# Kernel optimization log

Measured on AMD Instinct MI355X. Metric: run time of the kernel, lower is better.

The kernel has to match this reference:

```python
import jax, jax.numpy as jnp
import numpy as np

N_NODES = 20000   # N
N_EDGES = 320000  # E (avg degree 16)
T_STEPS = 16      # T
IN_FEATS = 1      # F
HG = 64           # hidden_g
HT = 128          # hidden_t
LN_EPS = 1e-5


def _layer_norm(x, g, b):
    mu = jnp.mean(x, axis=-1, keepdims=True)
    var = jnp.mean((x - mu) ** 2, axis=-1, keepdims=True)
    return (x - mu) * jax.lax.rsqrt(var + LN_EPS) * g + b


def setup_inputs() -> dict:
    key = jax.random.key(0)
    k = jax.random.split(key, 16)
    r = lambda i, shape, s: jax.random.normal(k[i], shape, jnp.float32) * s
    return dict(
        x_seq=jax.random.normal(k[0], (1, T_STEPS, N_NODES, IN_FEATS), jnp.float32),
        edge_index=jax.random.randint(k[1], (2, N_EDGES), 0, N_NODES, dtype=jnp.int32),
        # SAGEConv layer 0: lin_l (aggregated neighbors, has bias) + lin_r (root)
        W_l0=r(2, (IN_FEATS, HG), 0.5), W_r0=r(3, (IN_FEATS, HG), 0.5), b0=jnp.zeros((HG,), jnp.float32),
        ln0_g=jnp.ones((HG,), jnp.float32), ln0_b=jnp.zeros((HG,), jnp.float32),
        # SAGEConv layer 1
        W_l1=r(4, (HG, HG), 0.1), W_r1=r(5, (HG, HG), 0.1), b1=jnp.zeros((HG,), jnp.float32),
        ln1_g=jnp.ones((HG,), jnp.float32), ln1_b=jnp.zeros((HG,), jnp.float32),
        # GRU (torch layout: gates r,z,n stacked along first dim)
        gru_Wih=r(6, (3 * HT, HG), 0.05), gru_Whh=r(7, (3 * HT, HT), 0.05),
        gru_bih=jnp.zeros((3 * HT,), jnp.float32), gru_bhh=jnp.zeros((3 * HT,), jnp.float32),
        # head
        head_W=r(8, (HT, 1), 0.05), head_b=jnp.zeros((1,), jnp.float32),
    )


def reference(x_seq, edge_index, W_l0, W_r0, b0, ln0_g, ln0_b,
              W_l1, W_r1, b1, ln1_g, ln1_b,
              gru_Wih, gru_Whh, gru_bih, gru_bhh, head_W, head_b):
    src, dst = edge_index[0], edge_index[1]
    # in-degree for mean aggregation (clamped to 1, like PyG mean aggr on isolated nodes)
    deg = jnp.clip(jax.ops.segment_sum(jnp.ones((N_EDGES,), jnp.float32), dst,
                                       num_segments=N_NODES), 1.0)[:, None]

    def sage(x, Wl, Wr, b):
        # mean over incoming neighbors, then lin_l(aggr) + lin_r(root)
        agg = jax.ops.segment_sum(x[src], dst, num_segments=N_NODES) / deg
        return agg @ Wl + x @ Wr + b

    def stack(xt):  # xt: (N, F) -> (N, HG); dropout is identity in eval mode
        h = jax.nn.relu(_layer_norm(sage(xt, W_l0, W_r0, b0), ln0_g, ln0_b))
        h = jax.nn.relu(_layer_norm(sage(h, W_l1, W_r1, b1), ln1_g, ln1_b))
        return h

    X = x_seq[0]  # (T, N, F), B == 1
    # scan over timesteps (matches the per-t Python loop, bounds peak memory)
    _, H = jax.lax.scan(lambda c, xt: (c, stack(xt)), None, X)  # H: (T, N, HG)

    def gru_step(h, xt):  # torch GRU cell; batch = N nodes
        gi = xt @ gru_Wih.T + gru_bih
        gh = h @ gru_Whh.T + gru_bhh
        ir, iz, inn = jnp.split(gi, 3, axis=-1)
        hr, hz, hn = jnp.split(gh, 3, axis=-1)
        r = jax.nn.sigmoid(ir + hr)
        z = jax.nn.sigmoid(iz + hz)
        n = jnp.tanh(inn + r * hn)
        return (1.0 - z) * n + z * h, None

    h0 = jnp.zeros((N_NODES, HT), x_seq.dtype)
    hT, _ = jax.lax.scan(gru_step, h0, H)
    y = (hT @ head_W + head_b)[:, 0]  # (N,)
    return y
```

## Files before the change

### kernel.cpp

```cpp
#include <hip/hip_runtime.h>
#include <math.h>

#define NN 20000
#define NE 320000
#define TS 16
#define HG 64
#define HTT 128
#define NG 384
#define LN_EPS 1e-5f
#define ASTR 1032

typedef __attribute__((ext_vector_type(8))) _Float16 f16x8;
typedef __attribute__((ext_vector_type(4))) float f32x4;

__device__ __forceinline__ float wave_sum64(float v) {
  #pragma unroll
  for (int off = 32; off > 0; off >>= 1) v += __shfl_xor(v, off, 64);
  return v;
}
__device__ __forceinline__ float quad_sum16(float v) {
  #pragma unroll
  for (int off = 1; off < 16; off <<= 1) v += __shfl_xor(v, off, 64);
  return v;
}
__device__ __forceinline__ float fast_sigmoid(float x) {
  return __builtin_amdgcn_rcpf(1.f + __expf(-x));
}
__device__ __forceinline__ float fast_tanh(float x) {
  float e = __expf(-2.f * fabsf(x));
  float th = (1.f - e) * __builtin_amdgcn_rcpf(1.f + e);
  return copysignf(th, x);
}

__global__ void k_init(int* cnt) {
  int i = blockIdx.x * blockDim.x + threadIdx.x;
  if (i < NN) cnt[i] = 0;
}

__global__ void k_hist(const int* __restrict__ dst, int* cnt) {
  int e = blockIdx.x * blockDim.x + threadIdx.x;
  if (e < NE) atomicAdd(&cnt[dst[e]], 1);
}

__global__ void k_scan(int* cnt, int* row_ptr, float* deg_inv) {
  __shared__ int s[1024];
  const int PER = 20;
  int tid = threadIdx.x;
  int base = tid * PER;
  int vloc[PER], dloc[PER];
  int sum = 0;
  #pragma unroll
  for (int j = 0; j < PER; j++) {
    int n = base + j;
    int d = (n < NN) ? cnt[n] : 0;
    vloc[j] = sum;
    dloc[j] = d;
    sum += d;
  }
  s[tid] = sum;
  __syncthreads();
  for (int off = 1; off < 1024; off <<= 1) {
    int t = (tid >= off) ? s[tid - off] : 0;
    __syncthreads();
    s[tid] += t;
    __syncthreads();
  }
  int excl = s[tid] - sum;
  #pragma unroll
  for (int j = 0; j < PER; j++) {
    int n = base + j;
    if (n < NN) {
      int rp = excl + vloc[j];
      row_ptr[n] = rp;
      cnt[n] = rp;
      int d = dloc[j];
      deg_inv[n] = 1.0f / (float)((d > 1) ? d : 1);
    }
  }
  if (tid == 1023) row_ptr[NN] = s[1023];
}

__global__ void k_fill(const int* __restrict__ src, const int* __restrict__ dst,
                       int* cursor, int* col) {
  int e = blockIdx.x * blockDim.x + threadIdx.x;
  if (e < NE) {
    int p = atomicAdd(&cursor[dst[e]], 1);
    col[p] = src[e];
  }
}

__global__ void k_cvt_f16(const float* __restrict__ w, _Float16* __restrict__ o, int n) {
  int i = blockIdx.x * blockDim.x + threadIdx.x;
  if (i < n) o[i] = (_Float16)w[i];
}

__global__ void k_cvt_sagef16(const float* __restrict__ Wl1, const float* __restrict__ Wr1,
                              _Float16* __restrict__ hi, _Float16* __restrict__ lo) {
  int i = blockIdx.x * blockDim.x + threadIdx.x;
  if (i < HG * 128) {
    int n = i >> 7, k = i & 127;
    float x = (k < HG) ? Wl1[k * HG + n] : Wr1[(k - HG) * HG + n];
    _Float16 h = (_Float16)x;
    hi[i] = h;
    lo[i] = (_Float16)(x - (float)h);
  }
}

__global__ void k_moments(const float* __restrict__ Wl0, const float* __restrict__ Wr0,
                          const float* __restrict__ b0, const float* __restrict__ g0,
                          const float* __restrict__ be0, float* __restrict__ P) {
  int f = threadIdx.x;
  float u = Wl0[f], v = Wr0[f], c = b0[f], g = g0[f];
  float um = wave_sum64(u) * (1.f / 64.f);
  float vm = wave_sum64(v) * (1.f / 64.f);
  float cm = wave_sum64(c) * (1.f / 64.f);
  float uc = u - um, vc = v - vm, cc = c - cm;
  float muu = wave_sum64(uc * uc) * (1.f / 64.f);
  float mvv = wave_sum64(vc * vc) * (1.f / 64.f);
  float mcc = wave_sum64(cc * cc) * (1.f / 64.f);
  float muv = wave_sum64(uc * vc) * (1.f / 64.f);
  float muc = wave_sum64(uc * cc) * (1.f / 64.f);
  float mvc = wave_sum64(vc * cc) * (1.f / 64.f);
  P[f] = uc * g; P[64 + f] = vc * g; P[128 + f] = cc * g; P[192 + f] = be0[f];
  if (f == 0) {
    P[256] = muu; P[257] = mvv; P[258] = mcc;
    P[259] = muv; P[260] = muc; P[261] = mvc;
  }
}

__global__ void k_xt(const float* __restrict__ x_seq, float* __restrict__ xT) {
  int i = blockIdx.x * 256 + threadIdx.x;
  int t = i / NN, n = i - t * NN;
  xT[n * 16 + t] = x_seq[i];
}

__global__ __launch_bounds__(256) void k_agg0(
    const float* __restrict__ xT,
    const int* __restrict__ row_ptr, const int* __restrict__ col,
    const float* __restrict__ deg_inv,
    float* __restrict__ agg0) {
  int lane = threadIdx.x & 63;
  int n = blockIdx.x * 4 + (threadIdx.x >> 6);
  int grp = lane >> 4, tl = lane & 15;
  int beg = row_ptr[n];
  int deg = row_ptr[n + 1] - beg;
  float s0 = 0.f, s1 = 0.f;
  int iters = (deg + 7) >> 3;
  for (int it = 0; it < iters; it++) {
    int e0 = it * 8 + grp, e1 = it * 8 + 4 + grp;
    bool v0 = e0 < deg, v1 = e1 < deg;
    int i0 = v0 ? e0 : 0, i1 = v1 ? e1 : 0;
    int c0 = col[beg + i0];
    int c1 = col[beg + i1];
    float x0 = xT[c0 * 16 + tl];
    float x1 = xT[c1 * 16 + tl];
    s0 += v0 ? x0 : 0.f;
    s1 += v1 ? x1 : 0.f;
  }
  float s = s0 + s1;
  s += __shfl_xor(s, 16, 64);
  s += __shfl_xor(s, 32, 64);
  if (grp == 0) agg0[n * 16 + tl] = s * deg_inv[n];
}

__global__ __launch_bounds__(256) void k_h0(
    const float* __restrict__ xT, const float* __restrict__ agg0,
    const float* __restrict__ P,
    _Float16* __restrict__ h0r) {
  int i = blockIdx.x * 256 + threadIdx.x;
  int n = i >> 7, rem = i & 127;
  int t = rem >> 3, f8 = (rem & 7) * 8;
  float a = agg0[n * 16 + t];
  float x = xT[n * 16 + t];
  float muu = P[256], mvv = P[257], mcc = P[258];
  float muv = P[259], muc = P[260], mvc = P[261];
  float var = a * a * muu + x * x * mvv + mcc
            + 2.f * (a * x * muv + a * muc + x * mvc);
  float rstd = rsqrtf(var + LN_EPS);
  f16x8 o;
  #pragma unroll
  for (int j = 0; j < 8; j++) {
    int f = f8 + j;
    float d = a * P[f] + x * P[64 + f] + P[128 + f];
    o[j] = (_Float16)fmaxf(d * rstd + P[192 + f], 0.f);
  }
  *(f16x8*)&h0r[(size_t)n * 1024 + t * 64 + f8] = o;
}

__global__ __launch_bounds__(256) void k_sage_fused(
    const _Float16* __restrict__ h0r,
    const int* __restrict__ row_ptr, const int* __restrict__ col,
    const float* __restrict__ deg_inv,
    const _Float16* __restrict__ Wchi, const _Float16* __restrict__ Wclo,
    const float* __restrict__ b1, const float* __restrict__ g1, const float* __restrict__ be1,
    _Float16* __restrict__ Ht_all) {
  __shared__ _Float16 aggL[16 * ASTR];
  int tid = threadIdx.x;
  int lane = tid & 63, wave = tid >> 6;
  int col16 = lane & 15, quad = lane >> 4;
  int m0 = blockIdx.x * 16;

  for (int i = 0; i < 4; i++) {
    int nl = wave * 4 + i;
    int n = m0 + nl;
    int beg = row_ptr[n];
    int deg = row_ptr[n + 1] - beg;
    const f16x8 z = {0,0,0,0,0,0,0,0};
    f16x8 aH0 = z, aH1 = z, aH2 = z, aH3 = z;
    f16x8 aL0 = z, aL1 = z, aL2 = z, aL3 = z;
    int e = 0;
    for (; e + 8 <= deg; e += 8) {
      int c0 = col[beg + e + 0], c1 = col[beg + e + 1];
      int c2 = col[beg + e + 2], c3 = col[beg + e + 3];
      int c4 = col[beg + e + 4], c5 = col[beg + e + 5];
      int c6 = col[beg + e + 6], c7 = col[beg + e + 7];
      const f16x8* p0 = (const f16x8*)(h0r + (size_t)c0 * 1024);
      const f16x8* p1 = (const f16x8*)(h0r + (size_t)c1 * 1024);
      const f16x8* p2 = (const f16x8*)(h0r + (size_t)c2 * 1024);
      const f16x8* p3 = (const f16x8*)(h0r + (size_t)c3 * 1024);
      const f16x8* p4 = (const f16x8*)(h0r + (size_t)c4 * 1024);
      const f16x8* p5 = (const f16x8*)(h0r + (size_t)c5 * 1024);
      const f16x8* p6 = (const f16x8*)(h0r + (size_t)c6 * 1024);
      const f16x8* p7 = (const f16x8*)(h0r + (size_t)c7 * 1024);
      f16x8 d0a = p0[lane], d0b = p0[lane + 64];
      f16x8 d1a = p1[lane], d1b = p1[lane + 64];
      f16x8 d2a = p2[lane], d2b = p2[lane + 64];
      f16x8 d3a = p3[lane], d3b = p3[lane + 64];
      f16x8 d4a = p4[lane], d4b = p4[lane + 64];
      f16x8 d5a = p5[lane], d5b = p5[lane + 64];
      f16x8 d6a = p6[lane], d6b = p6[lane + 64];
      f16x8 d7a = p7[lane], d7b = p7[lane + 64];
      aH0 += d0a; aL0 += d0b;
      aH1 += d1a; aL1 += d1b;
      aH2 += d2a; aL2 += d2b;
      aH3 += d3a; aL3 += d3b;
      aH0 += d4a; aL0 += d4b;
      aH1 += d5a; aL1 += d5b;
      aH2 += d6a; aL2 += d6b;
      aH3 += d7a; aL3 += d7b;
    }
    for (; e + 4 <= deg; e += 4) {
      int c0 = col[beg + e + 0], c1 = col[beg + e + 1];
      int c2 = col[beg + e + 2], c3 = col[beg + e + 3];
      const f16x8* p0 = (const f16x8*)(h0r + (size_t)c0 * 1024);
      const f16x8* p1 = (const f16x8*)(h0r + (size_t)c1 * 1024);
      const f16x8* p2 = (const f16x8*)(h0r + (size_t)c2 * 1024);
      const f16x8* p3 = (const f16x8*)(h0r + (size_t)c3 * 1024);
      f16x8 d0a = p0[lane], d0b = p0[lane + 64];
      f16x8 d1a = p1[lane], d1b = p1[lane + 64];
      f16x8 d2a = p2[lane], d2b = p2[lane + 64];
      f16x8 d3a = p3[lane], d3b = p3[lane + 64];
      aH0 += d0a; aL0 += d0b;
      aH1 += d1a; aL1 += d1b;
      aH2 += d2a; aL2 += d2b;
      aH3 += d3a; aL3 += d3b;
    }
    for (; e < deg; e++) {
      int c = col[beg + e];
      const f16x8* p = (const f16x8*)(h0r + (size_t)c * 1024);
      aH0 += p[lane]; aL0 += p[lane + 64];
    }
    float di = deg_inv[n];
    f16x8 o0, o1;
    #pragma unroll
    for (int j = 0; j < 8; j++) {
      o0[j] = (_Float16)((((float)aH0[j] + (float)aH1[j]) +
                          ((float)aH2[j] + (float)aH3[j])) * di);
      o1[j] = (_Float16)((((float)aL0[j] + (float)aL1[j]) +
                          ((float)aL2[j] + (float)aL3[j])) * di);
    }
    *(f16x8*)&aggL[nl * ASTR + lane * 8] = o0;
    *(f16x8*)&aggL[nl * ASTR + 512 + lane * 8] = o1;
  }
  __syncthreads();

  for (int ts = 0; ts < 4; ts++) {
    int t = wave * 4 + ts;
    f32x4 acc[4];
    #pragma unroll
    for (int nt = 0; nt < 4; nt++) acc[nt] = (f32x4){0.f, 0.f, 0.f, 0.f};

    #pragma unroll
    for (int kk = 0; kk < 2; kk++) {
      f16x8 ah = *(const f16x8*)&aggL[col16 * ASTR + t * 64 + kk * 32 + quad * 8];
      #pragma unroll
      for (int nt = 0; nt < 4; nt++) {
        int nf = nt * 16 + col16;
        f16x8 bh = *(const f16x8*)&Wchi[nf * 128 + kk * 32 + quad * 8];
        f16x8 bl = *(const f16x8*)&Wclo[nf * 128 + kk * 32 + quad * 8];
        acc[nt] = __builtin_amdgcn_mfma_f32_16x16x32_f16(ah, bh, acc[nt], 0, 0, 0);
        acc[nt] = __builtin_amdgcn_mfma_f32_16x16x32_f16(ah, bl, acc[nt], 0, 0, 0);
      }
    }
    #pragma unroll
    for (int kk = 0; kk < 2; kk++) {
      f16x8 ah = *(const f16x8*)&h0r[(size_t)(m0 + col16) * 1024 + t * 64 + kk * 32 + quad * 8];
      #pragma unroll
      for (int nt = 0; nt < 4; nt++) {
        int nf = nt * 16 + col16;
        f16x8 bh = *(const f16x8*)&Wchi[nf * 128 + 64 + kk * 32 + quad * 8];
        f16x8 bl = *(const f16x8*)&Wclo[nf * 128 + 64 + kk * 32 + quad * 8];
        acc[nt] = __builtin_amdgcn_mfma_f32_16x16x32_f16(ah, bh, acc[nt], 0, 0, 0);
        acc[nt] = __builtin_amdgcn_mfma_f32_16x16x32_f16(ah, bl, acc[nt], 0, 0, 0);
      }
    }

    float bias[4], gg[4], bb[4];
    #pragma unroll
    for (int nt = 0; nt < 4; nt++) {
      int nf = nt * 16 + col16;
      bias[nt] = b1[nf]; gg[nt] = g1[nf]; bb[nt] = be1[nf];
    }
    #pragma unroll
    for (int r = 0; r < 4; r++) {
      float v[4];
      #pragma unroll
      for (int nt = 0; nt < 4; nt++) v[nt] = acc[nt][r] + bias[nt];
      float s = (v[0] + v[1]) + (v[2] + v[3]);
      float mu = quad_sum16(s) * (1.f / 64.f);
      float sq = 0.f;
      #pragma unroll
      for (int nt = 0; nt < 4; nt++) { v[nt] -= mu; sq += v[nt] * v[nt]; }
      float var = quad_sum16(sq) * (1.f / 64.f);
      float rstd = rsqrtf(var + LN_EPS);
      int m = m0 + quad * 4 + r;
      size_t base = ((size_t)t * NN + m) * HG;
      #pragma unroll
      for (int nt = 0; nt < 4; nt++) {
        float o = fmaxf(v[nt] * rstd * gg[nt] + bb[nt], 0.f);
        Ht_all[base + nt * 16 + col16] = (_Float16)o;
      }
    }
  }
}

__global__ __launch_bounds__(256, 2) void k_gru_all(
    const _Float16* __restrict__ Ht_all,
    const _Float16* __restrict__ WihF,
    const _Float16* __restrict__ WhhF,
    const float* __restrict__ bih, const float* __restrict__ bhh,
    const float* __restrict__ headW, const float* __restrict__ headb,
    float* __restrict__ out) {
  __shared__ _Float16 WihL[NG * 64];
  __shared__ _Float16 hL[2][32 * 128];
  __shared__ float yL[4][32];

  int tid = threadIdx.x;
  int lane = tid & 63, wave = tid >> 6;
  int col16 = lane & 15, quad = lane >> 4;
  int m0 = blockIdx.x * 32;
  int gb = 2 * wave;

  for (int i = tid; i < NG * 8; i += 256) {
    int g = i >> 3, k8 = i & 7;
    *(f16x8*)&WihL[g * 64 + ((k8 + g) & 7) * 8] = *(const f16x8*)&WihF[g * 64 + k8 * 8];
  }
  for (int i = tid; i < 2 * 32 * 128; i += 256) hL[0][i] = (_Float16)0.f;

  int gts[6];
  #pragma unroll
  for (int t6 = 0; t6 < 6; t6++)
    gts[t6] = (t6 < 2) ? (gb + t6) : (t6 < 4) ? (8 + gb + t6 - 2) : (16 + gb + t6 - 4);

  f16x8 wgh[4][6];
  #pragma unroll
  for (int kk = 0; kk < 4; kk++)
    #pragma unroll
    for (int t6 = 0; t6 < 6; t6++)
      wgh[kk][t6] = *(const f16x8*)&WhhF[(size_t)(gts[t6] * 16 + col16) * HTT + kk * 32 + quad * 8];

  int jj[2]; float bR[2], bZ[2], bNi[2], bNh[2], hw[2];
  int waddr[2][4][2];
  #pragma unroll
  for (int js = 0; js < 2; js++) {
    int j = (gb + js) * 16 + col16;
    jj[js] = j;
    bR[js]  = bih[j] + bhh[j];
    bZ[js]  = bih[HTT + j] + bhh[HTT + j];
    bNi[js] = bih[2 * HTT + j];
    bNh[js] = bhh[2 * HTT + j];
    hw[js]  = headW[j];
    #pragma unroll
    for (int mt = 0; mt < 2; mt++)
      #pragma unroll
      for (int r = 0; r < 4; r++) {
        int row = mt * 16 + quad * 4 + r;
        waddr[mt][r][js] = row * 128 + (((j >> 3) + row) & 15) * 8 + (j & 7);
      }
  }
  float hreg[2][4][2];
  #pragma unroll
  for (int mt = 0; mt < 2; mt++)
    #pragma unroll
    for (int r = 0; r < 4; r++) { hreg[mt][r][0] = 0.f; hreg[mt][r][1] = 0.f; }

  size_t aoff[2][2];
  #pragma unroll
  for (int kk = 0; kk < 2; kk++)
    #pragma unroll
    for (int mt = 0; mt < 2; mt++)
      aoff[kk][mt] = (size_t)(m0 + mt * 16 + col16) * HG + kk * 32 + quad * 8;

  __syncthreads();

  for (int t = 0; t < TS; t++) {
    const _Float16* hcur = hL[t & 1];
    _Float16* hnxt = hL[(t + 1) & 1];

    f32x4 acc[8][2];
    #pragma unroll
    for (int a = 0; a < 8; a++) {
      acc[a][0] = (f32x4){0.f, 0.f, 0.f, 0.f};
      acc[a][1] = (f32x4){0.f, 0.f, 0.f, 0.f};
    }

    const _Float16* AH = Ht_all + (size_t)t * NN * HG;
    f16x8 gah[2][2];
    #pragma unroll
    for (int kk = 0; kk < 2; kk++)
      #pragma unroll
      for (int mt = 0; mt < 2; mt++)
        gah[kk][mt] = *(const f16x8*)&AH[aoff[kk][mt]];

    #pragma unroll
    for (int kk = 0; kk < 4; kk++) {
      f16x8 ah[2];
      #pragma unroll
      for (int mt = 0; mt < 2; mt++) {
        int row = mt * 16 + col16;
        int k8 = kk * 4 + quad;
        ah[mt] = *(const f16x8*)&hcur[row * 128 + ((k8 + row) & 15) * 8];
      }
      #pragma unroll
      for (int t6 = 0; t6 < 6; t6++) {
        int ai = (t6 < 4) ? t6 : t6 + 2;
        #pragma unroll
        for (int mt = 0; mt < 2; mt++)
          acc[ai][mt] = __builtin_amdgcn_mfma_f32_16x16x32_f16(ah[mt], wgh[kk][t6], acc[ai][mt], 0, 0, 0);
      }
    }
    #pragma unroll
    for (int kk = 0; kk < 2; kk++) {
      #pragma unroll
      for (int t6 = 0; t6 < 6; t6++) {
        int g = gts[t6] * 16 + col16;
        int k8 = kk * 4 + quad;
        f16x8 b = *(const f16x8*)&WihL[g * 64 + ((k8 + g) & 7) * 8];
        #pragma unroll
        for (int mt = 0; mt < 2; mt++)
          acc[t6][mt] = __builtin_amdgcn_mfma_f32_16x16x32_f16(gah[kk][mt], b, acc[t6][mt], 0, 0, 0);
      }
    }

    #pragma unroll
    for (int mt = 0; mt < 2; mt++) {
      #pragma unroll
      for (int r = 0; r < 4; r++) {
        #pragma unroll
        for (int js = 0; js < 2; js++) {
          float R  = acc[0 + js][mt][r] + bR[js];
          float Z  = acc[2 + js][mt][r] + bZ[js];
          float Ni = acc[4 + js][mt][r] + bNi[js];
          float Nh = acc[6 + js][mt][r] + bNh[js];
          float rg = fast_sigmoid(R);
          float zg = fast_sigmoid(Z);
          float nn = fast_tanh(Ni + rg * Nh);
          float hn = nn + zg * (hreg[mt][r][js] - nn);
          hreg[mt][r][js] = hn;
          hnxt[waddr[mt][r][js]] = (_Float16)hn;
        }
      }
    }
    __syncthreads();
  }

  #pragma unroll
  for (int mt = 0; mt < 2; mt++) {
    #pragma unroll
    for (int r = 0; r < 4; r++) {
      float py = hreg[mt][r][0] * hw[0] + hreg[mt][r][1] * hw[1];
      py = quad_sum16(py);
      if (col16 == 0) yL[wave][mt * 16 + quad * 4 + r] = py;
    }
  }
  __syncthreads();
  if (tid < 32)
    out[m0 + tid] = yL[0][tid] + yL[1][tid] + yL[2][tid] + yL[3][tid] + headb[0];
}

extern "C" void kernel_launch(void* const* d_in, const int* in_sizes, int n_in,
                              void* d_out, int out_size, void* d_ws, size_t ws_size,
                              hipStream_t stream) {
  const float* x_seq = (const float*)d_in[0];
  const int*   edge  = (const int*)d_in[1];
  const float* Wl0   = (const float*)d_in[2];
  const float* Wr0   = (const float*)d_in[3];
  const float* b0    = (const float*)d_in[4];
  const float* g0    = (const float*)d_in[5];
  const float* be0   = (const float*)d_in[6];
  const float* Wl1   = (const float*)d_in[7];
  const float* Wr1   = (const float*)d_in[8];
  const float* b1    = (const float*)d_in[9];
  const float* g1    = (const float*)d_in[10];
  const float* be1   = (const float*)d_in[11];
  const float* Wih   = (const float*)d_in[12];
  const float* Whh   = (const float*)d_in[13];
  const float* bih   = (const float*)d_in[14];
  const float* bhh   = (const float*)d_in[15];
  const float* headW = (const float*)d_in[16];
  const float* headb = (const float*)d_in[17];
  float* out = (float*)d_out;

  const int* srcp = edge;
  const int* dstp = edge + NE;

  char* ws = (char*)d_ws;
  size_t off = 0;
  auto alloc = [&](size_t bytes) -> void* {
    void* p = ws + off;
    off += (bytes + 255) & ~(size_t)255;
    return p;
  };
  int*   cnt     = (int*)alloc(NN * 4);
  int*   row_ptr = (int*)alloc((NN + 1) * 4);
  int*   col     = (int*)alloc(NE * 4);
  float* deg_inv = (float*)alloc(NN * 4);
  float* xT      = (float*)alloc((size_t)NN * TS * 4);
  float* agg0    = (float*)alloc((size_t)NN * TS * 4);
  float* P       = (float*)alloc(512 * 4);
  _Float16* h0r  = (_Float16*)alloc((size_t)NN * 1024 * 2);
  _Float16* Ht_all = (_Float16*)alloc((size_t)TS * NN * HG * 2);
  _Float16* WihF = (_Float16*)alloc((size_t)NG * HG * 2);
  _Float16* WhhF = (_Float16*)alloc((size_t)NG * HTT * 2);
  _Float16* Wchi = (_Float16*)alloc((size_t)HG * 128 * 2);
  _Float16* Wclo = (_Float16*)alloc((size_t)HG * 128 * 2);
  (void)ws_size; (void)in_sizes; (void)n_in; (void)out_size;

  k_init<<<(NN + 255) / 256, 256, 0, stream>>>(cnt);
  k_hist<<<(NE + 255) / 256, 256, 0, stream>>>(dstp, cnt);
  k_scan<<<1, 1024, 0, stream>>>(cnt, row_ptr, deg_inv);
  k_fill<<<(NE + 255) / 256, 256, 0, stream>>>(srcp, dstp, cnt, col);
  k_cvt_f16<<<(NG * HG + 255) / 256, 256, 0, stream>>>(Wih, WihF, NG * HG);
  k_cvt_f16<<<(NG * HTT + 255) / 256, 256, 0, stream>>>(Whh, WhhF, NG * HTT);
  k_cvt_sagef16<<<(HG * 128 + 255) / 256, 256, 0, stream>>>(Wl1, Wr1, Wchi, Wclo);
  k_moments<<<1, 64, 0, stream>>>(Wl0, Wr0, b0, g0, be0, P);

  k_xt<<<NN * TS / 256, 256, 0, stream>>>(x_seq, xT);
  k_agg0<<<NN / 4, 256, 0, stream>>>(xT, row_ptr, col, deg_inv, agg0);
  k_h0<<<NN * 128 / 256, 256, 0, stream>>>(xT, agg0, P, h0r);
  k_sage_fused<<<NN / 16, 256, 0, stream>>>(h0r, row_ptr, col, deg_inv,
                                            Wchi, Wclo, b1, g1, be1, Ht_all);
  k_gru_all<<<NN / 32, 256, 0, stream>>>(Ht_all, WihF, WhhF, bih, bhh,
                                         headW, headb, out);
}
```

Measured before the change: 407.0 us.

## Merge setup kernels and fuse layer-0 aggregation with h0 layer-norm

Folds the counter init, weight conversions, moments computation and x transpose into one grid-stride setup kernel, removing several small launches. Fuses the layer-0 neighbor aggregation with the h0 layer-norm/ReLU, so the agg0 buffer is no longer written and read back and values pass between lanes by shuffle. Also adds a launch_bounds occupancy hint of 4 to the fused SAGE kernel, which may constrain registers and cause spills.

```diff
diff --git a/kernel.cpp b/kernel.cpp
--- a/kernel.cpp
+++ b/kernel.cpp
@@ -32,9 +32,51 @@
   return copysignf(th, x);
 }
 
-__global__ void k_init(int* cnt) {
-  int i = blockIdx.x * blockDim.x + threadIdx.x;
-  if (i < NN) cnt[i] = 0;
+__global__ __launch_bounds__(256) void k_setup(
+    const float* __restrict__ x_seq, float* __restrict__ xT,
+    const float* __restrict__ Wih, _Float16* __restrict__ WihF,
+    const float* __restrict__ Whh, _Float16* __restrict__ WhhF,
+    const float* __restrict__ Wl1, const float* __restrict__ Wr1,
+    _Float16* __restrict__ Wchi, _Float16* __restrict__ Wclo,
+    const float* __restrict__ Wl0, const float* __restrict__ Wr0,
+    const float* __restrict__ b0, const float* __restrict__ g0,
+    const float* __restrict__ be0, float* __restrict__ P,
+    int* __restrict__ cnt) {
+  int gid = blockIdx.x * 256 + threadIdx.x;
+  int stride = gridDim.x * 256;
+  for (int i = gid; i < NN * TS; i += stride) {
+    int t = i / NN, n = i - t * NN;
+    xT[n * 16 + t] = x_seq[i];
+  }
+  for (int i = gid; i < NG * HG; i += stride) WihF[i] = (_Float16)Wih[i];
+  for (int i = gid; i < NG * HTT; i += stride) WhhF[i] = (_Float16)Whh[i];
+  for (int i = gid; i < HG * 128; i += stride) {
+    int n = i >> 7, k = i & 127;
+    float x = (k < HG) ? Wl1[k * HG + n] : Wr1[(k - HG) * HG + n];
+    _Float16 h = (_Float16)x;
+    Wchi[i] = h;
+    Wclo[i] = (_Float16)(x - (float)h);
+  }
+  for (int i = gid; i < NN; i += stride) cnt[i] = 0;
+  if (blockIdx.x == 0 && threadIdx.x < 64) {
+    int f = threadIdx.x;
+    float u = Wl0[f], v = Wr0[f], c = b0[f], g = g0[f];
+    float um = wave_sum64(u) * (1.f / 64.f);
+    float vm = wave_sum64(v) * (1.f / 64.f);
+    float cm = wave_sum64(c) * (1.f / 64.f);
+    float uc = u - um, vc = v - vm, cc = c - cm;
+    float muu = wave_sum64(uc * uc) * (1.f / 64.f);
+    float mvv = wave_sum64(vc * vc) * (1.f / 64.f);
+    float mcc = wave_sum64(cc * cc) * (1.f / 64.f);
+    float muv = wave_sum64(uc * vc) * (1.f / 64.f);
+    float muc = wave_sum64(uc * cc) * (1.f / 64.f);
+    float mvc = wave_sum64(vc * cc) * (1.f / 64.f);
+    P[f] = uc * g; P[64 + f] = vc * g; P[128 + f] = cc * g; P[192 + f] = be0[f];
+    if (f == 0) {
+      P[256] = muu; P[257] = mvv; P[258] = mcc;
+      P[259] = muv; P[260] = muc; P[261] = mvc;
+    }
+  }
 }
 
 __global__ void k_hist(const int* __restrict__ dst, int* cnt) {
@@ -89,56 +131,12 @@
   }
 }
 
-__global__ void k_cvt_f16(const float* __restrict__ w, _Float16* __restrict__ o, int n) {
-  int i = blockIdx.x * blockDim.x + threadIdx.x;
-  if (i < n) o[i] = (_Float16)w[i];
-}
-
-__global__ void k_cvt_sagef16(const float* __restrict__ Wl1, const float* __restrict__ Wr1,
-                              _Float16* __restrict__ hi, _Float16* __restrict__ lo) {
-  int i = blockIdx.x * blockDim.x + threadIdx.x;
-  if (i < HG * 128) {
-    int n = i >> 7, k = i & 127;
-    float x = (k < HG) ? Wl1[k * HG + n] : Wr1[(k - HG) * HG + n];
-    _Float16 h = (_Float16)x;
-    hi[i] = h;
-    lo[i] = (_Float16)(x - (float)h);
-  }
-}
-
-__global__ void k_moments(const float* __restrict__ Wl0, const float* __restrict__ Wr0,
-                          const float* __restrict__ b0, const float* __restrict__ g0,
-                          const float* __restrict__ be0, float* __restrict__ P) {
-  int f = threadIdx.x;
-  float u = Wl0[f], v = Wr0[f], c = b0[f], g = g0[f];
-  float um = wave_sum64(u) * (1.f / 64.f);
-  float vm = wave_sum64(v) * (1.f / 64.f);
-  float cm = wave_sum64(c) * (1.f / 64.f);
-  float uc = u - um, vc = v - vm, cc = c - cm;
-  float muu = wave_sum64(uc * uc) * (1.f / 64.f);
-  float mvv = wave_sum64(vc * vc) * (1.f / 64.f);
-  float mcc = wave_sum64(cc * cc) * (1.f / 64.f);
-  float muv = wave_sum64(uc * vc) * (1.f / 64.f);
-  float muc = wave_sum64(uc * cc) * (1.f / 64.f);
-  float mvc = wave_sum64(vc * cc) * (1.f / 64.f);
-  P[f] = uc * g; P[64 + f] = vc * g; P[128 + f] = cc * g; P[192 + f] = be0[f];
-  if (f == 0) {
-    P[256] = muu; P[257] = mvv; P[258] = mcc;
-    P[259] = muv; P[260] = muc; P[261] = mvc;
-  }
-}
-
-__global__ void k_xt(const float* __restrict__ x_seq, float* __restrict__ xT) {
-  int i = blockIdx.x * 256 + threadIdx.x;
-  int t = i / NN, n = i - t * NN;
-  xT[n * 16 + t] = x_seq[i];
-}
-
-__global__ __launch_bounds__(256) void k_agg0(
+__global__ __launch_bounds__(256) void k_h0_fused(
     const float* __restrict__ xT,
     const int* __restrict__ row_ptr, const int* __restrict__ col,
     const float* __restrict__ deg_inv,
-    float* __restrict__ agg0) {
+    const float* __restrict__ P,
+    _Float16* __restrict__ h0r) {
   int lane = threadIdx.x & 63;
   int n = blockIdx.x * 4 + (threadIdx.x >> 6);
   int grp = lane >> 4, tl = lane & 15;
@@ -160,34 +158,31 @@
   float s = s0 + s1;
   s += __shfl_xor(s, 16, 64);
   s += __shfl_xor(s, 32, 64);
-  if (grp == 0) agg0[n * 16 + tl] = s * deg_inv[n];
-}
-
-__global__ __launch_bounds__(256) void k_h0(
-    const float* __restrict__ xT, const float* __restrict__ agg0,
-    const float* __restrict__ P,
-    _Float16* __restrict__ h0r) {
-  int i = blockIdx.x * 256 + threadIdx.x;
-  int n = i >> 7, rem = i & 127;
-  int t = rem >> 3, f8 = (rem & 7) * 8;
-  float a = agg0[n * 16 + t];
-  float x = xT[n * 16 + t];
+  float aggv = s * deg_inv[n];
+  float xv = xT[n * 16 + tl];
   float muu = P[256], mvv = P[257], mcc = P[258];
   float muv = P[259], muc = P[260], mvc = P[261];
-  float var = a * a * muu + x * x * mvv + mcc
-            + 2.f * (a * x * muv + a * muc + x * mvc);
-  float rstd = rsqrtf(var + LN_EPS);
-  f16x8 o;
-  #pragma unroll
-  for (int j = 0; j < 8; j++) {
-    int f = f8 + j;
-    float d = a * P[f] + x * P[64 + f] + P[128 + f];
-    o[j] = (_Float16)fmaxf(d * rstd + P[192 + f], 0.f);
-  }
-  *(f16x8*)&h0r[(size_t)n * 1024 + t * 64 + f8] = o;
-}
-
-__global__ __launch_bounds__(256) void k_sage_fused(
+  #pragma unroll
+  for (int half = 0; half < 2; half++) {
+    int c = lane + half * 64;
+    int t = c >> 3, f8 = (c & 7) * 8;
+    float a = __shfl(aggv, t, 64);
+    float x = __shfl(xv, t, 64);
+    float var = a * a * muu + x * x * mvv + mcc
+              + 2.f * (a * x * muv + a * muc + x * mvc);
+    float rstd = rsqrtf(var + LN_EPS);
+    f16x8 o;
+    #pragma unroll
+    for (int j = 0; j < 8; j++) {
+      int f = f8 + j;
+      float d = a * P[f] + x * P[64 + f] + P[128 + f];
+      o[j] = (_Float16)fmaxf(d * rstd + P[192 + f], 0.f);
+    }
+    *(f16x8*)&h0r[(size_t)n * 1024 + c * 8] = o;
+  }
+}
+
+__global__ __launch_bounds__(256, 4) void k_sage_fused(
     const _Float16* __restrict__ h0r,
     const int* __restrict__ row_ptr, const int* __restrict__ col,
     const float* __restrict__ deg_inv,
@@ -526,7 +521,6 @@
   int*   col     = (int*)alloc(NE * 4);
   float* deg_inv = (float*)alloc(NN * 4);
   float* xT      = (float*)alloc((size_t)NN * TS * 4);
-  float* agg0    = (float*)alloc((size_t)NN * TS * 4);
   float* P       = (float*)alloc(512 * 4);
   _Float16* h0r  = (_Float16*)alloc((size_t)NN * 1024 * 2);
   _Float16* Ht_all = (_Float16*)alloc((size_t)TS * NN * HG * 2);
@@ -536,18 +530,13 @@
   _Float16* Wclo = (_Float16*)alloc((size_t)HG * 128 * 2);
   (void)ws_size; (void)in_sizes; (void)n_in; (void)out_size;
 
-  k_init<<<(NN + 255) / 256, 256, 0, stream>>>(cnt);
+  k_setup<<<1250, 256, 0, stream>>>(x_seq, xT, Wih, WihF, Whh, WhhF,
+                                    Wl1, Wr1, Wchi, Wclo,
+                                    Wl0, Wr0, b0, g0, be0, P, cnt);
   k_hist<<<(NE + 255) / 256, 256, 0, stream>>>(dstp, cnt);
   k_scan<<<1, 1024, 0, stream>>>(cnt, row_ptr, deg_inv);
   k_fill<<<(NE + 255) / 256, 256, 0, stream>>>(srcp, dstp, cnt, col);
-  k_cvt_f16<<<(NG * HG + 255) / 256, 256, 0, stream>>>(Wih, WihF, NG * HG);
-  k_cvt_f16<<<(NG * HTT + 255) / 256, 256, 0, stream>>>(Whh, WhhF, NG * HTT);
-  k_cvt_sagef16<<<(HG * 128 + 255) / 256, 256, 0, stream>>>(Wl1, Wr1, Wchi, Wclo);
-  k_moments<<<1, 64, 0, stream>>>(Wl0, Wr0, b0, g0, be0, P);
-
-  k_xt<<<NN * TS / 256, 256, 0, stream>>>(x_seq, xT);
-  k_agg0<<<NN / 4, 256, 0, stream>>>(xT, row_ptr, col, deg_inv, agg0);
-  k_h0<<<NN * 128 / 256, 256, 0, stream>>>(xT, agg0, P, h0r);
+  k_h0_fused<<<NN / 4, 256, 0, stream>>>(xT, row_ptr, col, deg_inv, P, h0r);
   k_sage_fused<<<NN / 16, 256, 0, stream>>>(h0r, row_ptr, col, deg_inv,
                                             Wchi, Wclo, b1, g1, be1, Ht_all);
   k_gru_all<<<NN / 32, 256, 0, stream>>>(Ht_all, WihF, WhhF, bih, bhh,
```

New measurement: 446.9 us. 1.1x slower.
